# Kernel tuning notes

Hardware: AMD Instinct MI355X
Metric: run time of the kernel (lower is better)

## Reference

```python
import jax, jax.numpy as jnp
import numpy as np

N_NODES = 100000
N_EDGES = 1600000
HID = 64
BN_EPS = 1e-5


def _glorot(key, shape):
    fan_in, fan_out = shape[0], shape[1]
    lim = np.sqrt(6.0 / (fan_in + fan_out))
    return jax.random.uniform(key, shape, jnp.float32, -lim, lim)


def setup_inputs() -> dict:
    key = jax.random.key(0)
    ks = jax.random.split(key, 16)
    inp = {
        "x": jax.random.normal(ks[0], (N_NODES, HID), jnp.float32),
        "edge_index": jax.random.randint(ks[1], (2, N_EDGES), 0, N_NODES, jnp.int64),
        "edge_attr": jax.random.normal(ks[2], (N_EDGES,), jnp.float32),
    }
    # per-layer GIN MLP params: Linear(in,hid) -> BN(hid) -> ReLU -> Linear(hid,out)
    for i in range(2):
        inp[f"W1_{i}"] = _glorot(ks[3 + 5 * i], (HID, HID))
        inp[f"b1_{i}"] = jnp.zeros((HID,), jnp.float32)
        inp[f"gamma_{i}"] = jnp.ones((HID,), jnp.float32)
        inp[f"beta_{i}"] = jnp.zeros((HID,), jnp.float32)
        inp[f"W2_{i}"] = _glorot(ks[4 + 5 * i], (HID, HID))
        inp[f"b2_{i}"] = jnp.zeros((HID,), jnp.float32)
    inp["Wjk"] = _glorot(ks[14], (3 * HID, HID))
    inp["bjk"] = jnp.zeros((HID,), jnp.float32)
    return inp


def _gin_conv(x, src, dst, W1, b1, gamma, beta, W2, b2):
    # GIN aggregation: (1 + eps) * x + sum_{j->i} x_j, eps = 0
    agg = jax.ops.segment_sum(x[src], dst, num_segments=N_NODES)  # [N, d]
    h = (x + agg) @ W1 + b1
    # BatchNorm1d over node dimension (training-style batch statistics)
    mean = jnp.mean(h, axis=0)
    var = jnp.var(h, axis=0)
    h = gamma * (h - mean) * jax.lax.rsqrt(var + BN_EPS) + beta
    h = jax.nn.relu(h)
    return h @ W2 + b2


def reference(x, edge_index, edge_attr,
              W1_0, b1_0, gamma_0, beta_0, W2_0, b2_0,
              W1_1, b1_1, gamma_1, beta_1, W2_1, b2_1,
              Wjk, bjk):
    # edge_attr is accepted but ignored (torch_geometric GINConv does not use it)
    src, dst = edge_index[0], edge_index[1]
    xs = [x]
    h = x
    params = [(W1_0, b1_0, gamma_0, beta_0, W2_0, b2_0),
              (W1_1, b1_1, gamma_1, beta_1, W2_1, b2_1)]
    for p in params:
        h = _gin_conv(h, src, dst, *p)
        h = jax.nn.relu(h)  # dropout p=0.0 is identity
        xs.append(h)
    return jnp.concatenate(xs, axis=-1) @ Wjk + bjk
```

## Files before the change

kernel.cpp:

```cpp
#include <hip/hip_runtime.h>

#define N_NODES 100000
#define N_EDGES 1600000
#define HID 64
#define BN_EPS 1e-5f

#define GATHER_BLOCKS (N_NODES / 32)

#define ROW_TILES (N_NODES / 16)
#define TPW1 4
#define G1_BLOCKS ((ROW_TILES + 4*TPW1 - 1) / (4*TPW1))
#define TPW2 2
#define G2_BLOCKS ((ROW_TILES + 4*TPW2 - 1) / (4*TPW2))

#define SR_BLOCKS 64

#define NB 391
#define MS_BLOCKS 1000
#define MS_EPB (N_EDGES / MS_BLOCKS)
#define MS_CNT (NB * MS_BLOCKS)
#define GS_CHUNK 512
#define GS_BLOCKS ((MS_CNT + GS_CHUNK - 1) / GS_CHUNK)

#define CVT_B 3125
#define WT_B 112
#define PREP_BLOCKS (CVT_B + WT_B + MS_BLOCKS)

typedef __bf16 bf16x8 __attribute__((ext_vector_type(8)));
typedef float  f32x4  __attribute__((ext_vector_type(4)));
typedef unsigned short u16x8 __attribute__((ext_vector_type(8)));

__device__ __forceinline__ float bf2f(unsigned short u) {
    return __uint_as_float(((unsigned)u) << 16);
}
__device__ __forceinline__ unsigned short f2bf_rne(float f) {
    unsigned u = __float_as_uint(f);
    u += 0x7FFFu + ((u >> 16) & 1u);
    return (unsigned short)(u >> 16);
}

__global__ __launch_bounds__(256) void prep_kernel(
        const float* __restrict__ x, unsigned short* __restrict__ xb,
        const float* __restrict__ Wjk,
        const float* __restrict__ W1_0, const float* __restrict__ W2_0,
        const float* __restrict__ W1_1, const float* __restrict__ W2_1,
        unsigned short* __restrict__ wjk_t,
        unsigned short* __restrict__ w1t_0, unsigned short* __restrict__ w2t_0,
        unsigned short* __restrict__ w1t_1, unsigned short* __restrict__ w2t_1,
        const int* __restrict__ dst, int* __restrict__ cnt) {
    __shared__ int h[NB];
    const int b = blockIdx.x;
    if (b < CVT_B) {
        size_t i = ((size_t)b * 256 + threadIdx.x) * 8;
        float4 a = *reinterpret_cast<const float4*>(x + i);
        float4 c = *reinterpret_cast<const float4*>(x + i + 4);
        ushort4 w0 = make_ushort4(f2bf_rne(a.x), f2bf_rne(a.y), f2bf_rne(a.z), f2bf_rne(a.w));
        ushort4 w1 = make_ushort4(f2bf_rne(c.x), f2bf_rne(c.y), f2bf_rne(c.z), f2bf_rne(c.w));
        *reinterpret_cast<ushort4*>(xb + i) = w0;
        *reinterpret_cast<ushort4*>(xb + i + 4) = w1;
    } else if (b < CVT_B + WT_B) {
        int i = (b - CVT_B) * 256 + threadIdx.x;
        if (i < 12288) {
            int c = i / 192, k = i - c * 192;
            wjk_t[i] = f2bf_rne(Wjk[k * 64 + c]);
        } else {
            int r = i - 12288;
            int which = r >> 12, rem = r & 4095;
            int c = rem >> 6, k = rem & 63;
            const float* W = (which == 0) ? W1_0 : (which == 1) ? W2_0
                           : (which == 2) ? W1_1 : W2_1;
            unsigned short* Wt = (which == 0) ? w1t_0 : (which == 1) ? w2t_0
                               : (which == 2) ? w1t_1 : w2t_1;
            Wt[rem] = f2bf_rne(W[k * 64 + c]);
        }
    } else {
        const int hb = b - CVT_B - WT_B;
        for (int i = threadIdx.x; i < NB; i += 256) h[i] = 0;
        __syncthreads();
        const int e0 = hb * MS_EPB;
        for (int e = e0 + threadIdx.x; e < e0 + MS_EPB; e += 256)
            atomicAdd(&h[dst[e] >> 8], 1);
        __syncthreads();
        for (int i = threadIdx.x; i < NB; i += 256)
            cnt[i * MS_BLOCKS + hb] = h[i];
    }
}

__global__ __launch_bounds__(256) void scan_partial_g(
        const int* __restrict__ in, int* __restrict__ out,
        int* __restrict__ bsums, int n) {
    __shared__ int sd[256];
    int t = threadIdx.x;
    int base = blockIdx.x * GS_CHUNK;
    int i0 = base + 2 * t, i1 = i0 + 1;
    int d0 = (i0 < n) ? in[i0] : 0;
    int d1 = (i1 < n) ? in[i1] : 0;
    sd[t] = d0 + d1;
    __syncthreads();
    for (int o = 1; o < 256; o <<= 1) {
        int v = (t >= o) ? sd[t - o] : 0;
        __syncthreads();
        sd[t] += v;
        __syncthreads();
    }
    int excl = sd[t] - (d0 + d1);
    if (i0 < n) out[i0] = excl;
    if (i1 < n) out[i1] = excl + d0;
    if (t == 255) bsums[blockIdx.x] = sd[255];
}

__global__ __launch_bounds__(256) void scan_bsums_kernel(int* __restrict__ bsums, int nb) {
    __shared__ int sd[256];
    int t = threadIdx.x;
    int v[4]; int s = 0;
#pragma unroll
    for (int k = 0; k < 4; ++k) {
        int i = t * 4 + k;
        v[k] = (i < nb) ? bsums[i] : 0;
        s += v[k];
    }
    sd[t] = s;
    __syncthreads();
    for (int o = 1; o < 256; o <<= 1) {
        int u = (t >= o) ? sd[t - o] : 0;
        __syncthreads();
        sd[t] += u;
        __syncthreads();
    }
    int run = sd[t] - s;
#pragma unroll
    for (int k = 0; k < 4; ++k) {
        int i = t * 4 + k;
        if (i < nb) bsums[i] = run;
        run += v[k];
    }
}

__global__ __launch_bounds__(256) void msplit_scatter_kernel(
        const int* __restrict__ src, const int* __restrict__ dst,
        const int* __restrict__ psum, const int* __restrict__ bsums,
        int* __restrict__ bucketed) {
    __shared__ int cur[NB];
    for (int i = threadIdx.x; i < NB; i += 256) {
        int idx = i * MS_BLOCKS + blockIdx.x;
        cur[i] = psum[idx] + bsums[idx >> 9];
    }
    __syncthreads();
    const int e0 = blockIdx.x * MS_EPB;
    for (int e = e0 + threadIdx.x; e < e0 + MS_EPB; e += 256) {
        int d = dst[e];
        int p = atomicAdd(&cur[d >> 8], 1);
        bucketed[p] = (src[e] << 8) | (d & 255);
    }
}

__global__ __launch_bounds__(256) void bucket_csr_kernel(
        const int* __restrict__ bucketed, const int* __restrict__ psum,
        const int* __restrict__ bsums,
        int* __restrict__ off, int* __restrict__ eidx) {
    const int j = blockIdx.x;
    const int t = threadIdx.x;
    __shared__ int deg[256];
    __shared__ int sd[256];
    __shared__ int base_s, size_s;
    if (t == 0) {
        int i0 = j * MS_BLOCKS;
        int b = psum[i0] + bsums[i0 >> 9];
        int nxt;
        if (j == NB - 1) nxt = N_EDGES;
        else {
            int i1 = (j + 1) * MS_BLOCKS;
            nxt = psum[i1] + bsums[i1 >> 9];
        }
        base_s = b; size_s = nxt - b;
    }
    deg[t] = 0;
    __syncthreads();
    const int base = base_s, size = size_s;
    const int nlo = j << 8;
    for (int i = t; i < size; i += 256)
        atomicAdd(&deg[(unsigned)bucketed[base + i] & 255u], 1);
    __syncthreads();
    int d0 = deg[t];
    sd[t] = d0;
    __syncthreads();
    for (int o = 1; o < 256; o <<= 1) {
        int v = (t >= o) ? sd[t - o] : 0;
        __syncthreads();
        sd[t] += v;
        __syncthreads();
    }
    int excl = sd[t] - d0;
    int g0 = nlo + t;
    if (g0 <= N_NODES) off[g0] = base + excl;
    __syncthreads();
    deg[t] = excl;
    __syncthreads();
    for (int i = t; i < size; i += 256) {
        unsigned e = (unsigned)bucketed[base + i];
        int p = atomicAdd(&deg[e & 255u], 1);
        eidx[base + p] = (int)(e >> 8);
    }
}

__global__ __launch_bounds__(256) void gather_kernel(
        const unsigned short* __restrict__ xb, const int* __restrict__ off,
        const int* __restrict__ eidx, unsigned short* __restrict__ aggb) {
    const int lane = threadIdx.x & 63;
    const int g    = lane >> 3;
    const int col  = (lane & 7) << 3;
    const int w    = threadIdx.x >> 6;
    const int n = blockIdx.x * 32 + w * 8 + g;

    const int beg = off[n], end = off[n + 1];
    bf16x8 s8 = *reinterpret_cast<const bf16x8*>(xb + (size_t)n * HID + col);
    float acc[8];
#pragma unroll
    for (int i = 0; i < 8; ++i) acc[i] = (float)s8[i];

    int j = beg;
    for (; j + 4 <= end; j += 4) {
        int s0 = eidx[j], s1 = eidx[j + 1], s2 = eidx[j + 2], s3 = eidx[j + 3];
        bf16x8 r0 = *reinterpret_cast<const bf16x8*>(xb + (size_t)s0 * HID + col);
        bf16x8 r1 = *reinterpret_cast<const bf16x8*>(xb + (size_t)s1 * HID + col);
        bf16x8 r2 = *reinterpret_cast<const bf16x8*>(xb + (size_t)s2 * HID + col);
        bf16x8 r3 = *reinterpret_cast<const bf16x8*>(xb + (size_t)s3 * HID + col);
#pragma unroll
        for (int i = 0; i < 8; ++i)
            acc[i] += ((float)r0[i] + (float)r1[i]) + ((float)r2[i] + (float)r3[i]);
    }
    for (; j < end; ++j) {
        int s0 = eidx[j];
        bf16x8 r0 = *reinterpret_cast<const bf16x8*>(xb + (size_t)s0 * HID + col);
#pragma unroll
        for (int i = 0; i < 8; ++i) acc[i] += (float)r0[i];
    }

    u16x8 o;
#pragma unroll
    for (int i = 0; i < 8; ++i) o[i] = f2bf_rne(acc[i]);
    *reinterpret_cast<u16x8*>(aggb + (size_t)n * HID + col) = o;
}

__global__ __launch_bounds__(256) void gemm1_mfma_kernel(
        const unsigned short* __restrict__ aggb, const unsigned short* __restrict__ W1t,
        const float* __restrict__ bias, unsigned short* __restrict__ hb,
        float* __restrict__ stats_partial) {
    const int lane = threadIdx.x & 63;
    const int l15 = lane & 15, lhi = lane >> 4;
    const int w = threadIdx.x >> 6;

    bf16x8 bfrag[2][4];
    float bs[4];
#pragma unroll
    for (int f = 0; f < 4; ++f) {
        const unsigned short* wp = W1t + (size_t)(f * 16 + l15) * 64 + lhi * 8;
        bfrag[0][f] = *reinterpret_cast<const bf16x8*>(wp);
        bfrag[1][f] = *reinterpret_cast<const bf16x8*>(wp + 32);
        bs[f] = bias[f * 16 + l15];
    }

    float ssum[4] = {0.f, 0.f, 0.f, 0.f}, ssq[4] = {0.f, 0.f, 0.f, 0.f};

    const int tile0 = (blockIdx.x * 4 + w) * TPW1;
#pragma unroll
    for (int tt = 0; tt < TPW1; ++tt) {
        const int tile = tile0 + tt;
        if (tile < ROW_TILES) {
            const int r0 = tile * 16;
            const size_t arow = (size_t)(r0 + l15) * 64 + lhi * 8;
            bf16x8 a0 = *reinterpret_cast<const bf16x8*>(aggb + arow);
            bf16x8 a1 = *reinterpret_cast<const bf16x8*>(aggb + arow + 32);
            f32x4 acc[4];
#pragma unroll
            for (int f = 0; f < 4; ++f) acc[f] = (f32x4){bs[f], bs[f], bs[f], bs[f]};
#pragma unroll
            for (int f = 0; f < 4; ++f) {
                acc[f] = __builtin_amdgcn_mfma_f32_16x16x32_bf16(a0, bfrag[0][f], acc[f], 0, 0, 0);
                acc[f] = __builtin_amdgcn_mfma_f32_16x16x32_bf16(a1, bfrag[1][f], acc[f], 0, 0, 0);
            }
#pragma unroll
            for (int f = 0; f < 4; ++f)
#pragma unroll
                for (int i = 0; i < 4; ++i) {
                    hb[(size_t)(r0 + lhi * 4 + i) * 64 + f * 16 + l15] = f2bf_rne(acc[f][i]);
                    ssum[f] += acc[f][i];
                    ssq[f]  += acc[f][i] * acc[f][i];
                }
        }
    }

    __shared__ float red[2][4][256];
#pragma unroll
    for (int f = 0; f < 4; ++f) {
        red[0][f][threadIdx.x] = ssum[f];
        red[1][f][threadIdx.x] = ssq[f];
    }
    __syncthreads();
    if (threadIdx.x < 64) {
        int c = threadIdx.x, f = c >> 4, p = c & 15;
        float s = 0.f, q = 0.f;
#pragma unroll
        for (int u = 0; u < 16; ++u) {
            int t = (u >> 2) * 64 + (u & 3) * 16 + p;
            s += red[0][f][t];
            q += red[1][f][t];
        }
        stats_partial[(size_t)blockIdx.x * 128 + c]      = s;
        stats_partial[(size_t)blockIdx.x * 128 + 64 + c] = q;
    }
}

__global__ __launch_bounds__(256) void stats_reduce_kernel(
        const float* __restrict__ in, float* __restrict__ out, int nrows) {
    __shared__ float red[256];
    const int c = threadIdx.x & 127;
    const int half = threadIdx.x >> 7;
    float s = 0.f;
    for (int r = blockIdx.x + half * SR_BLOCKS; r < nrows; r += 2 * SR_BLOCKS)
        s += in[(size_t)r * 128 + c];
    red[threadIdx.x] = s;
    __syncthreads();
    if (half == 0)
        out[(size_t)blockIdx.x * 128 + c] = red[c] + red[128 + c];
}

__global__ __launch_bounds__(256) void bn_gemm_mfma_kernel(
        const unsigned short* __restrict__ hb, const unsigned short* __restrict__ W2t,
        const float* __restrict__ bias, const float* __restrict__ scale,
        const float* __restrict__ shift, unsigned short* __restrict__ outb) {
    const int lane = threadIdx.x & 63;
    const int l15 = lane & 15, lhi = lane >> 4;
    const int w = threadIdx.x >> 6;

    bf16x8 bfrag[2][4];
    float bs[4];
#pragma unroll
    for (int f = 0; f < 4; ++f) {
        const unsigned short* wp = W2t + (size_t)(f * 16 + l15) * 64 + lhi * 8;
        bfrag[0][f] = *reinterpret_cast<const bf16x8*>(wp);
        bfrag[1][f] = *reinterpret_cast<const bf16x8*>(wp + 32);
        bs[f] = bias[f * 16 + l15];
    }
    float sc[2][8], sh[2][8];
#pragma unroll
    for (int t = 0; t < 2; ++t)
#pragma unroll
        for (int j = 0; j < 8; ++j) {
            int k = t * 32 + lhi * 8 + j;
            sc[t][j] = scale[k];
            sh[t][j] = shift[k];
        }

    const int tile0 = (blockIdx.x * 4 + w) * TPW2;
#pragma unroll
    for (int tt = 0; tt < TPW2; ++tt) {
        const int tile = tile0 + tt;
        if (tile >= ROW_TILES) return;
        const int r0 = tile * 16;
        f32x4 acc[4];
#pragma unroll
        for (int f = 0; f < 4; ++f) acc[f] = (f32x4){bs[f], bs[f], bs[f], bs[f]};
#pragma unroll
        for (int t = 0; t < 2; ++t) {
            const unsigned short* hp = hb + (size_t)(r0 + l15) * 64 + t * 32 + lhi * 8;
            bf16x8 raw = *reinterpret_cast<const bf16x8*>(hp);
            bf16x8 a;
#pragma unroll
            for (int j = 0; j < 8; ++j)
                a[j] = (__bf16)fmaxf(fmaf(sc[t][j], (float)raw[j], sh[t][j]), 0.f);
#pragma unroll
            for (int f = 0; f < 4; ++f)
                acc[f] = __builtin_amdgcn_mfma_f32_16x16x32_bf16(a, bfrag[t][f], acc[f], 0, 0, 0);
        }
#pragma unroll
        for (int f = 0; f < 4; ++f)
#pragma unroll
            for (int i = 0; i < 4; ++i)
                outb[(size_t)(r0 + lhi * 4 + i) * 64 + f * 16 + l15] =
                    f2bf_rne(fmaxf(acc[f][i], 0.f));
    }
}

#define LT_STRIDE 88
__global__ __launch_bounds__(256) void bn_gemm_jumphead_kernel(
        const unsigned short* __restrict__ hb, const unsigned short* __restrict__ W2t,
        const float* __restrict__ bias2, const float* __restrict__ scale,
        const float* __restrict__ shift,
        const unsigned short* __restrict__ xb, const unsigned short* __restrict__ h1b,
        const unsigned short* __restrict__ Wt, const float* __restrict__ bjk,
        float* __restrict__ out) {
    __shared__ unsigned short lt[4][16 * LT_STRIDE];
    const int lane = threadIdx.x & 63;
    const int l15 = lane & 15, lhi = lane >> 4;
    const int w = threadIdx.x >> 6;

    bf16x8 b2frag[2][4];
    float bs2[4];
#pragma unroll
    for (int f = 0; f < 4; ++f) {
        const unsigned short* wp = W2t + (size_t)(f * 16 + l15) * 64 + lhi * 8;
        b2frag[0][f] = *reinterpret_cast<const bf16x8*>(wp);
        b2frag[1][f] = *reinterpret_cast<const bf16x8*>(wp + 32);
        bs2[f] = bias2[f * 16 + l15];
    }
    float sc[2][8], sh[2][8];
#pragma unroll
    for (int t = 0; t < 2; ++t)
#pragma unroll
        for (int j = 0; j < 8; ++j) {
            int k = t * 32 + lhi * 8 + j;
            sc[t][j] = scale[k];
            sh[t][j] = shift[k];
        }
    bf16x8 bjfrag[6][4];
    float bsj[4];
#pragma unroll
    for (int f = 0; f < 4; ++f) {
        const unsigned short* wp = Wt + (size_t)(f * 16 + l15) * 192 + lhi * 8;
#pragma unroll
        for (int t = 0; t < 6; ++t)
            bjfrag[t][f] = *reinterpret_cast<const bf16x8*>(wp + t * 32);
        bsj[f] = bjk[f * 16 + l15];
    }

    const int tile0 = (blockIdx.x * 4 + w) * TPW2;
#pragma unroll
    for (int tt = 0; tt < TPW2; ++tt) {
        const int tile = tile0 + tt;
        if (tile >= ROW_TILES) return;
        const int r0 = tile * 16;

        f32x4 acc2[4];
#pragma unroll
        for (int f = 0; f < 4; ++f) acc2[f] = (f32x4){bs2[f], bs2[f], bs2[f], bs2[f]};
#pragma unroll
        for (int t = 0; t < 2; ++t) {
            const unsigned short* hp = hb + (size_t)(r0 + l15) * 64 + t * 32 + lhi * 8;
            bf16x8 raw = *reinterpret_cast<const bf16x8*>(hp);
            bf16x8 a;
#pragma unroll
            for (int j = 0; j < 8; ++j)
                a[j] = (__bf16)fmaxf(fmaf(sc[t][j], (float)raw[j], sh[t][j]), 0.f);
#pragma unroll
            for (int f = 0; f < 4; ++f)
                acc2[f] = __builtin_amdgcn_mfma_f32_16x16x32_bf16(a, b2frag[t][f], acc2[f], 0, 0, 0);
        }
#pragma unroll
        for (int f = 0; f < 4; ++f)
#pragma unroll
            for (int i = 0; i < 4; ++i)
                lt[w][(lhi * 4 + i) * LT_STRIDE + f * 16 + l15] =
                    f2bf_rne(fmaxf(acc2[f][i], 0.f));
        bf16x8 a4 = *reinterpret_cast<const bf16x8*>(&lt[w][l15 * LT_STRIDE + lhi * 8]);
        bf16x8 a5 = *reinterpret_cast<const bf16x8*>(&lt[w][l15 * LT_STRIDE + 32 + lhi * 8]);

        const size_t arow = (size_t)(r0 + l15) * 64 + lhi * 8;
        bf16x8 a0 = *reinterpret_cast<const bf16x8*>(xb + arow);
        bf16x8 a1 = *reinterpret_cast<const bf16x8*>(xb + arow + 32);
        bf16x8 a2 = *reinterpret_cast<const bf16x8*>(h1b + arow);
        bf16x8 a3 = *reinterpret_cast<const bf16x8*>(h1b + arow + 32);
        f32x4 accj[4];
#pragma unroll
        for (int f = 0; f < 4; ++f) accj[f] = (f32x4){bsj[f], bsj[f], bsj[f], bsj[f]};
#pragma unroll
        for (int f = 0; f < 4; ++f) {
            accj[f] = __builtin_amdgcn_mfma_f32_16x16x32_bf16(a0, bjfrag[0][f], accj[f], 0, 0, 0);
            accj[f] = __builtin_amdgcn_mfma_f32_16x16x32_bf16(a1, bjfrag[1][f], accj[f], 0, 0, 0);
            accj[f] = __builtin_amdgcn_mfma_f32_16x16x32_bf16(a2, bjfrag[2][f], accj[f], 0, 0, 0);
            accj[f] = __builtin_amdgcn_mfma_f32_16x16x32_bf16(a3, bjfrag[3][f], accj[f], 0, 0, 0);
            accj[f] = __builtin_amdgcn_mfma_f32_16x16x32_bf16(a4, bjfrag[4][f], accj[f], 0, 0, 0);
            accj[f] = __builtin_amdgcn_mfma_f32_16x16x32_bf16(a5, bjfrag[5][f], accj[f], 0, 0, 0);
        }
#pragma unroll
        for (int f = 0; f < 4; ++f)
#pragma unroll
            for (int i = 0; i < 4; ++i)
                out[(size_t)(r0 + lhi * 4 + i) * 64 + f * 16 + l15] = accj[f][i];
    }
}

__global__ __launch_bounds__(1024) void bn_finalize_kernel(
        const float* __restrict__ stats_partial, int nblocks,
        const float* __restrict__ gamma, const float* __restrict__ beta,
        float* __restrict__ scale, float* __restrict__ shift) {
    __shared__ float red[2][1024];
    const int t = threadIdx.x;
    const int c = t & 63;
    const int chunk = t >> 6;
    float s = 0.f, q = 0.f;
    for (int b = chunk; b < nblocks; b += 16) {
        s += stats_partial[(size_t)b * 128 + c];
        q += stats_partial[(size_t)b * 128 + 64 + c];
    }
    red[0][t] = s;
    red[1][t] = q;
    __syncthreads();
    if (chunk == 0) {
        float ss = 0.f, qq = 0.f;
#pragma unroll
        for (int k = 0; k < 16; ++k) {
            ss += red[0][k * 64 + c];
            qq += red[1][k * 64 + c];
        }
        float mean = ss / (float)N_NODES;
        float var  = qq / (float)N_NODES - mean * mean;
        float scl  = gamma[c] * rsqrtf(var + BN_EPS);
        scale[c] = scl;
        shift[c] = beta[c] - mean * scl;
    }
}

extern "C" void kernel_launch(void* const* d_in, const int* in_sizes, int n_in,
                              void* d_out, int out_size, void* d_ws, size_t ws_size,
                              hipStream_t stream) {
    const float* x    = (const float*)d_in[0];
    const int*   ei   = (const int*)d_in[1];
    const int*   src  = ei;
    const int*   dst  = ei + N_EDGES;
    const float* W1_0 = (const float*)d_in[3];
    const float* b1_0 = (const float*)d_in[4];
    const float* g_0  = (const float*)d_in[5];
    const float* be_0 = (const float*)d_in[6];
    const float* W2_0 = (const float*)d_in[7];
    const float* b2_0 = (const float*)d_in[8];
    const float* W1_1 = (const float*)d_in[9];
    const float* b1_1 = (const float*)d_in[10];
    const float* g_1  = (const float*)d_in[11];
    const float* be_1 = (const float*)d_in[12];
    const float* W2_1 = (const float*)d_in[13];
    const float* b2_1 = (const float*)d_in[14];
    const float* Wjk  = (const float*)d_in[15];
    const float* bjk  = (const float*)d_in[16];

    const size_t FEAT = (size_t)N_NODES * HID;

    unsigned short* aggb = (unsigned short*)d_ws;
    unsigned short* hb   = aggb + FEAT;
    unsigned short* xb   = hb + FEAT;
    unsigned short* h1b  = xb + FEAT;
    int*   bucketed = (int*)(h1b + FEAT);
    float* stats  = (float*)(bucketed + N_EDGES);
    float* stats2 = stats + (size_t)G1_BLOCKS * 128;
    float* scale  = stats2 + (size_t)SR_BLOCKS * 128;
    float* shift  = scale + 64;
    int*   off   = (int*)(shift + 64);
    int*   eidx  = off + N_NODES + 2;
    int*   cnt   = eidx + N_EDGES;
    int*   psum  = cnt + MS_CNT;
    int*   bsums = psum + MS_CNT + 2;
    unsigned short* wjk_t = (unsigned short*)(bsums + 1024);
    unsigned short* w2t_0 = wjk_t + 64 * 192;
    unsigned short* w2t_1 = w2t_0 + 64 * 64;
    unsigned short* w1t_0 = w2t_1 + 64 * 64;
    unsigned short* w1t_1 = w1t_0 + 64 * 64;
    float* out   = (float*)d_out;

    prep_kernel<<<PREP_BLOCKS, 256, 0, stream>>>(
        x, xb, Wjk, W1_0, W2_0, W1_1, W2_1,
        wjk_t, w1t_0, w2t_0, w1t_1, w2t_1, dst, cnt);

    scan_partial_g<<<GS_BLOCKS, 256, 0, stream>>>(cnt, psum, bsums, MS_CNT);
    scan_bsums_kernel<<<1, 256, 0, stream>>>(bsums, GS_BLOCKS);
    msplit_scatter_kernel<<<MS_BLOCKS, 256, 0, stream>>>(src, dst, psum, bsums, bucketed);
    bucket_csr_kernel<<<NB, 256, 0, stream>>>(bucketed, psum, bsums, off, eidx);

    gather_kernel<<<GATHER_BLOCKS, 256, 0, stream>>>(xb, off, eidx, aggb);
    gemm1_mfma_kernel<<<G1_BLOCKS, 256, 0, stream>>>(aggb, w1t_0, b1_0, hb, stats);
    stats_reduce_kernel<<<SR_BLOCKS, 256, 0, stream>>>(stats, stats2, G1_BLOCKS);
    bn_finalize_kernel<<<1, 1024, 0, stream>>>(stats2, SR_BLOCKS, g_0, be_0, scale, shift);
    bn_gemm_mfma_kernel<<<G2_BLOCKS, 256, 0, stream>>>(hb, w2t_0, b2_0, scale, shift, h1b);

    gather_kernel<<<GATHER_BLOCKS, 256, 0, stream>>>(h1b, off, eidx, aggb);
    gemm1_mfma_kernel<<<G1_BLOCKS, 256, 0, stream>>>(aggb, w1t_1, b1_1, hb, stats);
    stats_reduce_kernel<<<SR_BLOCKS, 256, 0, stream>>>(stats, stats2, G1_BLOCKS);
    bn_finalize_kernel<<<1, 1024, 0, stream>>>(stats2, SR_BLOCKS, g_1, be_1, scale, shift);
    bn_gemm_jumphead_kernel<<<G2_BLOCKS, 256, 0, stream>>>(
        hb, w2t_1, b2_1, scale, shift, xb, h1b, wjk_t, bjk, out);
}
```

Baseline: 182.8 us.

## Recompute layer-0 first GEMM in BN kernel instead of storing h; unroll gather

For layer 0, the first GEMM kernel now only computes BN statistics and skips writing the hidden activations. The BN+second-GEMM kernel recomputes the first linear layer from the aggregated input, applies scale/shift/ReLU in registers, and transposes the result through LDS to feed the second MFMA. This removes a round trip of the hidden tensor through memory at the cost of repeating a small GEMM. Separately, the gather loop is unrolled to 8 neighbors with nontemporal index loads to raise memory-level parallelism.

After: 192.6 us. +5.4%, slower.

```diff
diff --git a/kernel.cpp b/kernel.cpp
--- a/kernel.cpp
+++ b/kernel.cpp
@@ -219,18 +219,44 @@
     for (int i = 0; i < 8; ++i) acc[i] = (float)s8[i];
 
     int j = beg;
-    for (; j + 4 <= end; j += 4) {
-        int s0 = eidx[j], s1 = eidx[j + 1], s2 = eidx[j + 2], s3 = eidx[j + 3];
+    for (; j + 8 <= end; j += 8) {
+        int s0 = __builtin_nontemporal_load(eidx + j);
+        int s1 = __builtin_nontemporal_load(eidx + j + 1);
+        int s2 = __builtin_nontemporal_load(eidx + j + 2);
+        int s3 = __builtin_nontemporal_load(eidx + j + 3);
+        int s4 = __builtin_nontemporal_load(eidx + j + 4);
+        int s5 = __builtin_nontemporal_load(eidx + j + 5);
+        int s6 = __builtin_nontemporal_load(eidx + j + 6);
+        int s7 = __builtin_nontemporal_load(eidx + j + 7);
         bf16x8 r0 = *reinterpret_cast<const bf16x8*>(xb + (size_t)s0 * HID + col);
         bf16x8 r1 = *reinterpret_cast<const bf16x8*>(xb + (size_t)s1 * HID + col);
         bf16x8 r2 = *reinterpret_cast<const bf16x8*>(xb + (size_t)s2 * HID + col);
         bf16x8 r3 = *reinterpret_cast<const bf16x8*>(xb + (size_t)s3 * HID + col);
+        bf16x8 r4 = *reinterpret_cast<const bf16x8*>(xb + (size_t)s4 * HID + col);
+        bf16x8 r5 = *reinterpret_cast<const bf16x8*>(xb + (size_t)s5 * HID + col);
+        bf16x8 r6 = *reinterpret_cast<const bf16x8*>(xb + (size_t)s6 * HID + col);
+        bf16x8 r7 = *reinterpret_cast<const bf16x8*>(xb + (size_t)s7 * HID + col);
+#pragma unroll
+        for (int i = 0; i < 8; ++i)
+            acc[i] += (((float)r0[i] + (float)r1[i]) + ((float)r2[i] + (float)r3[i]))
+                    + (((float)r4[i] + (float)r5[i]) + ((float)r6[i] + (float)r7[i]));
+    }
+    if (j + 4 <= end) {
+        int s0 = __builtin_nontemporal_load(eidx + j);
+        int s1 = __builtin_nontemporal_load(eidx + j + 1);
+        int s2 = __builtin_nontemporal_load(eidx + j + 2);
+        int s3 = __builtin_nontemporal_load(eidx + j + 3);
+        bf16x8 r0 = *reinterpret_cast<const bf16x8*>(xb + (size_t)s0 * HID + col);
+        bf16x8 r1 = *reinterpret_cast<const bf16x8*>(xb + (size_t)s1 * HID + col);
+        bf16x8 r2 = *reinterpret_cast<const bf16x8*>(xb + (size_t)s2 * HID + col);
+        bf16x8 r3 = *reinterpret_cast<const bf16x8*>(xb + (size_t)s3 * HID + col);
 #pragma unroll
         for (int i = 0; i < 8; ++i)
             acc[i] += ((float)r0[i] + (float)r1[i]) + ((float)r2[i] + (float)r3[i]);
+        j += 4;
     }
     for (; j < end; ++j) {
-        int s0 = eidx[j];
+        int s0 = __builtin_nontemporal_load(eidx + j);
         bf16x8 r0 = *reinterpret_cast<const bf16x8*>(xb + (size_t)s0 * HID + col);
 #pragma unroll
         for (int i = 0; i < 8; ++i) acc[i] += (float)r0[i];
@@ -242,6 +268,7 @@
     *reinterpret_cast<u16x8*>(aggb + (size_t)n * HID + col) = o;
 }
 
+template<bool WRITE_H>
 __global__ __launch_bounds__(256) void gemm1_mfma_kernel(
         const unsigned short* __restrict__ aggb, const unsigned short* __restrict__ W1t,
         const float* __restrict__ bias, unsigned short* __restrict__ hb,
@@ -283,7 +310,8 @@
             for (int f = 0; f < 4; ++f)
 #pragma unroll
                 for (int i = 0; i < 4; ++i) {
-                    hb[(size_t)(r0 + lhi * 4 + i) * 64 + f * 16 + l15] = f2bf_rne(acc[f][i]);
+                    if (WRITE_H)
+                        hb[(size_t)(r0 + lhi * 4 + i) * 64 + f * 16 + l15] = f2bf_rne(acc[f][i]);
                     ssum[f] += acc[f][i];
                     ssq[f]  += acc[f][i] * acc[f][i];
                 }
@@ -325,32 +353,32 @@
         out[(size_t)blockIdx.x * 128 + c] = red[c] + red[128 + c];
 }
 
+#define LT_STRIDE 88
 __global__ __launch_bounds__(256) void bn_gemm_mfma_kernel(
-        const unsigned short* __restrict__ hb, const unsigned short* __restrict__ W2t,
-        const float* __restrict__ bias, const float* __restrict__ scale,
+        const unsigned short* __restrict__ aggb, const unsigned short* __restrict__ W1t,
+        const float* __restrict__ bias1, const unsigned short* __restrict__ W2t,
+        const float* __restrict__ bias2, const float* __restrict__ scale,
         const float* __restrict__ shift, unsigned short* __restrict__ outb) {
+    __shared__ unsigned short lt[4][16 * LT_STRIDE];
     const int lane = threadIdx.x & 63;
     const int l15 = lane & 15, lhi = lane >> 4;
     const int w = threadIdx.x >> 6;
 
-    bf16x8 bfrag[2][4];
-    float bs[4];
+    bf16x8 w1frag[2][4], b2frag[2][4];
+    float b1C[4], scC[4], shC[4], bs2[4];
 #pragma unroll
     for (int f = 0; f < 4; ++f) {
-        const unsigned short* wp = W2t + (size_t)(f * 16 + l15) * 64 + lhi * 8;
-        bfrag[0][f] = *reinterpret_cast<const bf16x8*>(wp);
-        bfrag[1][f] = *reinterpret_cast<const bf16x8*>(wp + 32);
-        bs[f] = bias[f * 16 + l15];
-    }
-    float sc[2][8], sh[2][8];
-#pragma unroll
-    for (int t = 0; t < 2; ++t)
-#pragma unroll
-        for (int j = 0; j < 8; ++j) {
-            int k = t * 32 + lhi * 8 + j;
-            sc[t][j] = scale[k];
-            sh[t][j] = shift[k];
-        }
+        const unsigned short* wp1 = W1t + (size_t)(f * 16 + l15) * 64 + lhi * 8;
+        w1frag[0][f] = *reinterpret_cast<const bf16x8*>(wp1);
+        w1frag[1][f] = *reinterpret_cast<const bf16x8*>(wp1 + 32);
+        const unsigned short* wp2 = W2t + (size_t)(f * 16 + l15) * 64 + lhi * 8;
+        b2frag[0][f] = *reinterpret_cast<const bf16x8*>(wp2);
+        b2frag[1][f] = *reinterpret_cast<const bf16x8*>(wp2 + 32);
+        b1C[f] = bias1[f * 16 + l15];
+        scC[f] = scale[f * 16 + l15];
+        shC[f] = shift[f * 16 + l15];
+        bs2[f] = bias2[f * 16 + l15];
+    }
 
     const int tile0 = (blockIdx.x * 4 + w) * TPW2;
 #pragma unroll
@@ -358,20 +386,34 @@
         const int tile = tile0 + tt;
         if (tile >= ROW_TILES) return;
         const int r0 = tile * 16;
+
+        const size_t arow = (size_t)(r0 + l15) * 64 + lhi * 8;
+        bf16x8 a0 = *reinterpret_cast<const bf16x8*>(aggb + arow);
+        bf16x8 a1 = *reinterpret_cast<const bf16x8*>(aggb + arow + 32);
+        f32x4 hacc[4];
+#pragma unroll
+        for (int f = 0; f < 4; ++f) hacc[f] = (f32x4){b1C[f], b1C[f], b1C[f], b1C[f]};
+#pragma unroll
+        for (int f = 0; f < 4; ++f) {
+            hacc[f] = __builtin_amdgcn_mfma_f32_16x16x32_bf16(a0, w1frag[0][f], hacc[f], 0, 0, 0);
+            hacc[f] = __builtin_amdgcn_mfma_f32_16x16x32_bf16(a1, w1frag[1][f], hacc[f], 0, 0, 0);
+        }
+#pragma unroll
+        for (int f = 0; f < 4; ++f)
+#pragma unroll
+            for (int i = 0; i < 4; ++i)
+                lt[w][(lhi * 4 + i) * LT_STRIDE + f * 16 + l15] =
+                    f2bf_rne(fmaxf(fmaf(scC[f], hacc[f][i], shC[f]), 0.f));
+        bf16x8 ah0 = *reinterpret_cast<const bf16x8*>(&lt[w][l15 * LT_STRIDE + lhi * 8]);
+        bf16x8 ah1 = *reinterpret_cast<const bf16x8*>(&lt[w][l15 * LT_STRIDE + 32 + lhi * 8]);
+
         f32x4 acc[4];
 #pragma unroll
-        for (int f = 0; f < 4; ++f) acc[f] = (f32x4){bs[f], bs[f], bs[f], bs[f]};
-#pragma unroll
-        for (int t = 0; t < 2; ++t) {
-            const unsigned short* hp = hb + (size_t)(r0 + l15) * 64 + t * 32 + lhi * 8;
-            bf16x8 raw = *reinterpret_cast<const bf16x8*>(hp);
-            bf16x8 a;
-#pragma unroll
-            for (int j = 0; j < 8; ++j)
-                a[j] = (__bf16)fmaxf(fmaf(sc[t][j], (float)raw[j], sh[t][j]), 0.f);
-#pragma unroll
-            for (int f = 0; f < 4; ++f)
-                acc[f] = __builtin_amdgcn_mfma_f32_16x16x32_bf16(a, bfrag[t][f], acc[f], 0, 0, 0);
+        for (int f = 0; f < 4; ++f) acc[f] = (f32x4){bs2[f], bs2[f], bs2[f], bs2[f]};
+#pragma unroll
+        for (int f = 0; f < 4; ++f) {
+            acc[f] = __builtin_amdgcn_mfma_f32_16x16x32_bf16(ah0, b2frag[0][f], acc[f], 0, 0, 0);
+            acc[f] = __builtin_amdgcn_mfma_f32_16x16x32_bf16(ah1, b2frag[1][f], acc[f], 0, 0, 0);
         }
 #pragma unroll
         for (int f = 0; f < 4; ++f)
@@ -382,7 +424,6 @@
     }
 }
 
-#define LT_STRIDE 88
 __global__ __launch_bounds__(256) void bn_gemm_jumphead_kernel(
         const unsigned short* __restrict__ hb, const unsigned short* __restrict__ W2t,
         const float* __restrict__ bias2, const float* __restrict__ scale,
@@ -566,13 +607,14 @@
     bucket_csr_kernel<<<NB, 256, 0, stream>>>(bucketed, psum, bsums, off, eidx);
 
     gather_kernel<<<GATHER_BLOCKS, 256, 0, stream>>>(xb, off, eidx, aggb);
-    gemm1_mfma_kernel<<<G1_BLOCKS, 256, 0, stream>>>(aggb, w1t_0, b1_0, hb, stats);
+    gemm1_mfma_kernel<false><<<G1_BLOCKS, 256, 0, stream>>>(aggb, w1t_0, b1_0, hb, stats);
     stats_reduce_kernel<<<SR_BLOCKS, 256, 0, stream>>>(stats, stats2, G1_BLOCKS);
     bn_finalize_kernel<<<1, 1024, 0, stream>>>(stats2, SR_BLOCKS, g_0, be_0, scale, shift);
-    bn_gemm_mfma_kernel<<<G2_BLOCKS, 256, 0, stream>>>(hb, w2t_0, b2_0, scale, shift, h1b);
+    bn_gemm_mfma_kernel<<<G2_BLOCKS, 256, 0, stream>>>(
+        aggb, w1t_0, b1_0, w2t_0, b2_0, scale, shift, h1b);
 
     gather_kernel<<<GATHER_BLOCKS, 256, 0, stream>>>(h1b, off, eidx, aggb);
-    gemm1_mfma_kernel<<<G1_BLOCKS, 256, 0, stream>>>(aggb, w1t_1, b1_1, hb, stats);
+    gemm1_mfma_kernel<true><<<G1_BLOCKS, 256, 0, stream>>>(aggb, w1t_1, b1_1, hb, stats);
     stats_reduce_kernel<<<SR_BLOCKS, 256, 0, stream>>>(stats, stats2, G1_BLOCKS);
     bn_finalize_kernel<<<1, 1024, 0, stream>>>(stats2, SR_BLOCKS, g_1, be_1, scale, shift);
     bn_gemm_jumphead_kernel<<<G2_BLOCKS, 256, 0, stream>>>(
```
